# Performance work log

Hardware: AMD Instinct MI355X
Metric: run time of the kernel (lower is better)

## Reference

```python
import jax, jax.numpy as jnp
import numpy as np

PS = 3          # patch_size
ALPHA = 0.5     # alpha_0 (no step() calls -> stays at init value)
A_CUBIC = -0.75 # torch bicubic kernel coefficient


def _cubic_w(t):
    at = jnp.abs(t)
    w1 = ((A_CUBIC + 2.0) * at - (A_CUBIC + 3.0)) * at * at + 1.0
    w2 = A_CUBIC * (((at - 5.0) * at + 8.0) * at - 4.0)
    return jnp.where(at <= 1.0, w1, jnp.where(at < 2.0, w2, 0.0))


def _resize_axis(x, out_size, axis):
    # bicubic, align_corners=True, border-clamped (matches torch.nn.functional.interpolate)
    in_size = x.shape[axis]
    scale = (in_size - 1) / (out_size - 1)
    coords = jnp.arange(out_size, dtype=x.dtype) * jnp.asarray(scale, x.dtype)
    i0 = jnp.floor(coords)
    frac = coords - i0
    offs = jnp.arange(-1, 3)
    idx = jnp.clip(i0.astype(jnp.int32)[:, None] + offs[None, :], 0, in_size - 1)
    w = _cubic_w(frac[:, None] - offs[None, :].astype(x.dtype))  # [out,4]
    xm = jnp.moveaxis(x, axis, -1)
    vals = xm[..., idx]                      # [..., out, 4]
    out = jnp.einsum('...ot,ot->...o', vals, w)
    return jnp.moveaxis(out, -1, axis)


def _bicubic(x, out_h, out_w):
    return _resize_axis(_resize_axis(x, out_h, 2), out_w, 3)


def _unfold(x, ps=PS):
    # [B,C,H,W] -> [B, (H/ps)*(W/ps), C, ps, ps], row-major over (H-chunk, W-chunk)
    B, C, H, W = x.shape
    x = x.reshape(B, C, H // ps, ps, W // ps, ps)
    x = x.transpose(0, 2, 4, 1, 3, 5)
    return x.reshape(B, -1, C, ps, ps)


def _fold(p, C, H, W, ps=PS):
    B = p.shape[0]
    x = p.reshape(B, H // ps, W // ps, C, ps, ps)
    x = x.transpose(0, 3, 1, 4, 2, 5)
    return x.reshape(B, C, H, W)


def _g_database(tar, ps=PS):
    B, C, H, W = tar.shape
    scales = [tar, _bicubic(tar, H // 2, W // 2), _bicubic(tar, H // 4, W // 4)]
    patches = []
    for i in range(1, ps):
        for j in range(1, ps):
            for s in scales:
                h, w = s.shape[2], s.shape[3]
                if ps < min(h, w):
                    patches.append(_unfold(s[:, :, i:h - (ps - i), j:w - (ps - j)], ps))
    for s in scales:
        patches.append(_unfold(s, ps))
    return jnp.concatenate(patches, axis=1)  # [B, G, C, ps, ps]


def setup_inputs() -> dict:
    key = jax.random.key(0)
    k1, k2 = jax.random.split(key)
    inp = jax.random.uniform(k1, (2, 3, 144, 144), dtype=jnp.float32)
    tar = jax.random.uniform(k2, (2, 3, 144, 144), dtype=jnp.float32)
    return {"inp": inp, "tar": tar}


def reference(inp, tar):
    B, C, H, W = tar.shape
    ps = PS
    D = C * ps * ps
    ipf = _unfold(inp, ps).reshape(B, -1, D)   # [B,N,D]
    tpf = _unfold(tar, ps).reshape(B, -1, D)
    gf = _g_database(tar, ps).reshape(B, -1, D)  # [B,G,D]

    # nearest-candidate selection is done under no_grad in the original
    gf_s = jax.lax.stop_gradient(gf)
    tpf_s = jax.lax.stop_gradient(tpf)
    ipf_s = jax.lax.stop_gradient(ipf)
    gn = jnp.sum(gf_s * gf_s, axis=-1)  # [B,G]

    def sqdist(a):  # sum of squared diffs over D: [B,G,N]
        an = jnp.sum(a * a, axis=-1)
        return an[:, None, :] + gn[:, :, None] - 2.0 * jnp.einsum('bnd,bgd->bgn', a, gf_s)

    l = ALPHA * sqdist(tpf_s) + (1.0 - ALPHA) * sqdist(ipf_s)  # [B,G,N]
    index = jnp.argmin(l, axis=1)                              # [B,N]
    sel = jnp.take_along_axis(gf_s, index[..., None], axis=1)  # [B,N,D]

    loss_p = jnp.abs(ipf - sel)  # L1Loss(reduction='none')
    loss_img = _fold(loss_p.reshape(B, -1, C, ps, ps), C, H, W, ps)
    sel_img = _fold(sel.reshape(B, -1, C, ps, ps), C, H, W, ps)
    return loss_img.mean(), sel_img
```

## Files before the change

kernel.cpp:

```cpp
#include <hip/hip_runtime.h>
#include <math.h>

#define A_CUBIC (-0.75f)
#define NB 2
#define NC 3
#define HH 144
#define NPB 2304
#define GG 14460
#define DD 27
#define DP 28
#define GSPLIT 128
#define GTILE 113

typedef float v2f __attribute__((ext_vector_type(2)));

__constant__ int c_seg_start[15] = {0,2209,2738,2859,5068,5597,5718,7927,8456,8577,10786,11315,11436,13740,14316};
__constant__ int c_seg_gw[15]    = {47,23,11, 47,23,11, 47,23,11, 47,23,11, 48,24,12};
__constant__ int c_seg_oy[15]    = {1,1,1, 1,1,1, 2,2,2, 2,2,2, 0,0,0};
__constant__ int c_seg_ox[15]    = {1,1,1, 2,2,2, 1,1,1, 2,2,2, 0,0,0};
__constant__ int c_seg_src[15]   = {0,1,2, 0,1,2, 0,1,2, 0,1,2, 0,1,2};

__device__ __forceinline__ float cubicw(float t) {
    float at = fabsf(t);
    if (at <= 1.0f) return ((A_CUBIC + 2.0f) * at - (A_CUBIC + 3.0f)) * at * at + 1.0f;
    if (at < 2.0f)  return A_CUBIC * (((at - 5.0f) * at + 8.0f) * at - 4.0f);
    return 0.0f;
}

__global__ void prep_k(const float* __restrict__ tar, const float* __restrict__ inp,
                       float* __restrict__ s1, float* __restrict__ s2,
                       float* __restrict__ m, unsigned long long* __restrict__ best) {
    int t = blockIdx.x * 256 + threadIdx.x;
    const int total1 = NB * NC * 72 * 72;
    const int total2 = NB * NC * 36 * 36;
    if (t < total1 + total2) {
        float* dst; int O; int idx;
        if (t < total1) { dst = s1; O = 72; idx = t; }
        else            { dst = s2; O = 36; idx = t - total1; }
        int x  = idx % O;
        int y  = (idx / O) % O;
        int bc = idx / (O * O);
        const float* src = tar + (size_t)bc * HH * HH;
        float scale = (float)(143.0 / (double)(O - 1));
        float fy = (float)y * scale;
        float iyf = floorf(fy); float fry = fy - iyf; int iy = (int)iyf;
        float fx = (float)x * scale;
        float ixf = floorf(fx); float frx = fx - ixf; int ix = (int)ixf;
        float wy[4], wx[4];
        #pragma unroll
        for (int d = 0; d < 4; ++d) {
            wy[d] = cubicw(fry - (float)(d - 1));
            wx[d] = cubicw(frx - (float)(d - 1));
        }
        float acc = 0.0f;
        #pragma unroll
        for (int dx = 0; dx < 4; ++dx) {
            int cx = min(max(ix - 1 + dx, 0), HH - 1);
            float inner = 0.0f;
            #pragma unroll
            for (int dy = 0; dy < 4; ++dy) {
                int cy = min(max(iy - 1 + dy, 0), HH - 1);
                inner += wy[dy] * src[cy * HH + cx];
            }
            acc += wx[dx] * inner;
        }
        dst[idx] = acc;
    } else {
        int u = t - (total1 + total2);
        if (u >= NB * NPB) return;
        int b = u / NPB, n = u % NPB;
        int hc = n / 48, wc = n % 48;
        const float* ib = inp + (size_t)b * NC * HH * HH;
        const float* tb = tar + (size_t)b * NC * HH * HH;
        float* row = m + (size_t)u * DP;
        #pragma unroll
        for (int c = 0; c < 3; ++c)
            #pragma unroll
            for (int dy = 0; dy < 3; ++dy)
                #pragma unroll
                for (int dx = 0; dx < 3; ++dx) {
                    int off = (c * HH + hc * 3 + dy) * HH + wc * 3 + dx;
                    row[(c * 3 + dy) * 3 + dx] = ib[off] + tb[off];
                }
        row[27] = -1.0f;
        best[u] = 0ULL;
    }
}

__global__ void build_gf_k(const float* __restrict__ tar, const float* __restrict__ s1,
                           const float* __restrict__ s2, float* __restrict__ gf) {
    int t = blockIdx.x * 256 + threadIdx.x;
    if (t >= NB * GG) return;
    int b = t / GG, g = t % GG;
    int s = 0;
    #pragma unroll
    for (int k = 1; k < 15; ++k) if (g >= c_seg_start[k]) s = k;
    int p  = g - c_seg_start[s];
    int gw = c_seg_gw[s];
    int hc = p / gw, wc = p % gw;
    int oy = c_seg_oy[s], ox = c_seg_ox[s];
    int srci = c_seg_src[s];
    const float* img; int sz;
    if (srci == 0)      { img = tar; sz = 144; }
    else if (srci == 1) { img = s1;  sz = 72;  }
    else                { img = s2;  sz = 36;  }
    const float* base = img + (size_t)b * NC * sz * sz;
    int y0 = oy + hc * 3, x0 = ox + wc * 3;
    float acc = 0.0f;
    float* row = gf + (size_t)t * DP;
    #pragma unroll
    for (int c = 0; c < 3; ++c)
        #pragma unroll
        for (int dy = 0; dy < 3; ++dy)
            #pragma unroll
            for (int dx = 0; dx < 3; ++dx) {
                float v = base[((size_t)c * sz + y0 + dy) * sz + x0 + dx];
                row[(c * 3 + dy) * 3 + dx] = v;
                acc = fmaf(v, v, acc);
            }
    row[27] = acc;
}

__device__ __forceinline__ float dot28(const v2f mr[14], const v2f r[14]) {
    v2f a0 = {0.0f, 0.0f}, a1 = {0.0f, 0.0f};
    #pragma unroll
    for (int i = 0; i < 14; i += 2) {
        a0 = __builtin_elementwise_fma(mr[i],     r[i],     a0);
        a1 = __builtin_elementwise_fma(mr[i + 1], r[i + 1], a1);
    }
    v2f t = a0 + a1;
    return t.x + t.y;
}

__global__ __launch_bounds__(256, 8) void argmin_k(
        const float* __restrict__ gf, const float* __restrict__ m,
        unsigned long long* __restrict__ best) {
    int tid = threadIdx.x;
    int nblk = blockIdx.y;
    int b  = nblk / 9;
    int nn = nblk * 256 + tid;
    const v2f* mrow = (const v2f*)(m + (size_t)nn * DP);
    v2f mr[14];
    #pragma unroll
    for (int i = 0; i < 14; ++i) mr[i] = mrow[i];
    int g0 = blockIdx.x * GTILE;
    int g1 = min(g0 + GTILE, GG);
    const float* gfb = gf + (size_t)b * GG * DP;
    float bv = -3.0e38f; int bi = 0;

    v2f A[14], B[14];
    {
        const v2f* p = (const v2f*)(gfb + (size_t)g0 * DP);
        #pragma unroll
        for (int i = 0; i < 14; ++i) A[i] = p[i];
    }
    int g = g0;
    for (; g + 1 < g1; g += 2) {
        {
            const v2f* p = (const v2f*)(gfb + (size_t)(g + 1) * DP);
            #pragma unroll
            for (int i = 0; i < 14; ++i) B[i] = p[i];
        }
        float s = dot28(mr, A);
        if (s > bv) { bv = s; bi = g; }
        {
            const v2f* p = (const v2f*)(gfb + (size_t)(g + 2) * DP);
            #pragma unroll
            for (int i = 0; i < 14; ++i) A[i] = p[i];
        }
        float s2 = dot28(mr, B);
        if (s2 > bv) { bv = s2; bi = g + 1; }
    }
    if (g < g1) {
        float s = dot28(mr, A);
        if (s > bv) { bv = s; bi = g; }
    }
    unsigned u = __float_as_uint(bv);
    u ^= (unsigned)(((int)u >> 31)) | 0x80000000u;
    atomicMax(&best[nn], ((unsigned long long)u << 32) | (unsigned)(~bi));
}

__global__ void finalize_k(const float* __restrict__ gf,
                           const unsigned long long* __restrict__ best,
                           const float* __restrict__ inp,
                           float* __restrict__ out, float* __restrict__ lpart) {
    __shared__ float red[256];
    int t = blockIdx.x * 256 + threadIdx.x;
    float lsum = 0.0f;
    if (t < NB * NPB) {
        int b = t / NPB, n = t % NPB;
        unsigned long long pk = best[t];
        int bi = (int)(~(unsigned)(pk & 0xFFFFFFFFull));
        int hc = n / 48, wc = n % 48;
        const float* grow = gf + ((size_t)b * GG + bi) * DP;
        const float* ib   = inp + (size_t)b * NC * HH * HH;
        float* sel = out + 1 + (size_t)b * NC * HH * HH;
        #pragma unroll
        for (int c = 0; c < 3; ++c)
            #pragma unroll
            for (int dy = 0; dy < 3; ++dy)
                #pragma unroll
                for (int dx = 0; dx < 3; ++dx) {
                    int d = (c * 3 + dy) * 3 + dx;
                    float sv = grow[d];
                    int off = (c * HH + hc * 3 + dy) * HH + wc * 3 + dx;
                    sel[off] = sv;
                    lsum += fabsf(ib[off] - sv);
                }
    }
    red[threadIdx.x] = lsum;
    __syncthreads();
    for (int s = 128; s > 0; s >>= 1) {
        if (threadIdx.x < s) red[threadIdx.x] += red[threadIdx.x + s];
        __syncthreads();
    }
    if (threadIdx.x == 0) lpart[blockIdx.x] = red[0];
}

__global__ void sum_k(const float* __restrict__ lpart, float* __restrict__ out) {
    if (threadIdx.x == 0) {
        float s = 0.0f;
        for (int i = 0; i < 18; ++i) s += lpart[i];
        out[0] = s * (1.0f / 124416.0f);
    }
}

extern "C" void kernel_launch(void* const* d_in, const int* in_sizes, int n_in,
                              void* d_out, int out_size, void* d_ws, size_t ws_size,
                              hipStream_t stream) {
    const float* inp = (const float*)d_in[0];
    const float* tar = (const float*)d_in[1];
    float* out = (float*)d_out;
    float* ws  = (float*)d_ws;

    float* s1 = ws;
    float* s2 = s1 + 31104;
    float* gf = s2 + 7776;
    float* m  = gf + 809760;
    unsigned long long* best = (unsigned long long*)(m + 129024);
    float* lp = (float*)(best + 4608);

    prep_k    <<<(43488 + 255) / 256, 256, 0, stream>>>(tar, inp, s1, s2, m, best);
    build_gf_k<<<(28920 + 255) / 256, 256, 0, stream>>>(tar, s1, s2, gf);
    argmin_k  <<<dim3(GSPLIT, 18), 256, 0, stream>>>(gf, m, best);
    finalize_k<<<18, 256, 0, stream>>>(gf, best, inp, out, lp);
    sum_k     <<<1, 64, 0, stream>>>(lp, out);
}
```

Measured before the change: 79.94 us.

## Restructure argmin as shared-memory tiled GEMM with register blocking

The argmin kernel stops streaming each database row from global memory per thread. Instead, each block stages a 64-row query tile and 128-row database tiles, transposed, into LDS. Each thread then computes a 4x8 block of dot products from float4 LDS reads, keeps a running max per query, and a shared-memory reduction settles the winner per query before the atomic. To make the tiles uniform, the database is zero-padded to a multiple of 128 rows. This cuts redundant global/L1 traffic and raises arithmetic intensity, at the cost of block barriers and zero-padding rows that are only safe because real candidates always score higher.

```diff
diff --git a/kernel.cpp b/kernel.cpp
--- a/kernel.cpp
+++ b/kernel.cpp
@@ -7,12 +7,13 @@
 #define HH 144
 #define NPB 2304
 #define GG 14460
+#define GGP 14464
 #define DD 27
 #define DP 28
-#define GSPLIT 128
-#define GTILE 113
-
-typedef float v2f __attribute__((ext_vector_type(2)));
+#define NGT 113
+#define NSPLIT 16
+#define APAD 68
+#define BPAD 132
 
 __constant__ int c_seg_start[15] = {0,2209,2738,2859,5068,5597,5718,7927,8456,8577,10786,11315,11436,13740,14316};
 __constant__ int c_seg_gw[15]    = {47,23,11, 47,23,11, 47,23,11, 47,23,11, 48,24,12};
@@ -90,8 +91,14 @@
 __global__ void build_gf_k(const float* __restrict__ tar, const float* __restrict__ s1,
                            const float* __restrict__ s2, float* __restrict__ gf) {
     int t = blockIdx.x * 256 + threadIdx.x;
-    if (t >= NB * GG) return;
-    int b = t / GG, g = t % GG;
+    if (t >= NB * GGP) return;
+    int b = t / GGP, g = t % GGP;
+    float* row = gf + (size_t)t * DP;
+    if (g >= GG) {
+        #pragma unroll
+        for (int i = 0; i < DP; ++i) row[i] = 0.0f;
+        return;
+    }
     int s = 0;
     #pragma unroll
     for (int k = 1; k < 15; ++k) if (g >= c_seg_start[k]) s = k;
@@ -107,7 +114,6 @@
     const float* base = img + (size_t)b * NC * sz * sz;
     int y0 = oy + hc * 3, x0 = ox + wc * 3;
     float acc = 0.0f;
-    float* row = gf + (size_t)t * DP;
     #pragma unroll
     for (int c = 0; c < 3; ++c)
         #pragma unroll
@@ -121,63 +127,94 @@
     row[27] = acc;
 }
 
-__device__ __forceinline__ float dot28(const v2f mr[14], const v2f r[14]) {
-    v2f a0 = {0.0f, 0.0f}, a1 = {0.0f, 0.0f};
-    #pragma unroll
-    for (int i = 0; i < 14; i += 2) {
-        a0 = __builtin_elementwise_fma(mr[i],     r[i],     a0);
-        a1 = __builtin_elementwise_fma(mr[i + 1], r[i + 1], a1);
-    }
-    v2f t = a0 + a1;
-    return t.x + t.y;
-}
-
-__global__ __launch_bounds__(256, 8) void argmin_k(
+__global__ __launch_bounds__(256) void argmin_k(
         const float* __restrict__ gf, const float* __restrict__ m,
         unsigned long long* __restrict__ best) {
+    __shared__ __align__(16) float Al[28 * APAD];
+    __shared__ __align__(16) float Bl[28 * BPAD];
+    __shared__ float rv[64 * 17];
+    __shared__ int   ri[64 * 17];
     int tid = threadIdx.x;
-    int nblk = blockIdx.y;
-    int b  = nblk / 9;
-    int nn = nblk * 256 + tid;
-    const v2f* mrow = (const v2f*)(m + (size_t)nn * DP);
-    v2f mr[14];
-    #pragma unroll
-    for (int i = 0; i < 14; ++i) mr[i] = mrow[i];
-    int g0 = blockIdx.x * GTILE;
-    int g1 = min(g0 + GTILE, GG);
-    const float* gfb = gf + (size_t)b * GG * DP;
-    float bv = -3.0e38f; int bi = 0;
-
-    v2f A[14], B[14];
+    int tx = tid & 15;
+    int ty = tid >> 4;
+    int nt = blockIdx.y;
+    int n0 = nt * 64;
+    int b  = nt / 36;
+    int s  = blockIdx.x;
+    int t0 = (s * NGT) >> 4;
+    int t1 = ((s + 1) * NGT) >> 4;
+
     {
-        const v2f* p = (const v2f*)(gfb + (size_t)g0 * DP);
-        #pragma unroll
-        for (int i = 0; i < 14; ++i) A[i] = p[i];
-    }
-    int g = g0;
-    for (; g + 1 < g1; g += 2) {
+        const float* src = m + (size_t)n0 * DP;
+        for (int idx = tid; idx < 64 * DP; idx += 256) {
+            int r = idx / DP, k = idx - r * DP;
+            Al[k * APAD + r] = src[idx];
+        }
+    }
+
+    float bv[4]; int bi[4];
+    #pragma unroll
+    for (int i = 0; i < 4; ++i) { bv[i] = -3.0e38f; bi[i] = 0; }
+
+    const float* gbase = gf + (size_t)b * GGP * DP;
+    for (int t = t0; t < t1; ++t) {
+        __syncthreads();
         {
-            const v2f* p = (const v2f*)(gfb + (size_t)(g + 1) * DP);
-            #pragma unroll
-            for (int i = 0; i < 14; ++i) B[i] = p[i];
-        }
-        float s = dot28(mr, A);
-        if (s > bv) { bv = s; bi = g; }
-        {
-            const v2f* p = (const v2f*)(gfb + (size_t)(g + 2) * DP);
-            #pragma unroll
-            for (int i = 0; i < 14; ++i) A[i] = p[i];
-        }
-        float s2 = dot28(mr, B);
-        if (s2 > bv) { bv = s2; bi = g + 1; }
-    }
-    if (g < g1) {
-        float s = dot28(mr, A);
-        if (s > bv) { bv = s; bi = g; }
-    }
-    unsigned u = __float_as_uint(bv);
-    u ^= (unsigned)(((int)u >> 31)) | 0x80000000u;
-    atomicMax(&best[nn], ((unsigned long long)u << 32) | (unsigned)(~bi));
+            const float* src = gbase + (size_t)t * 128 * DP;
+            for (int idx = tid; idx < 128 * DP; idx += 256) {
+                int r = idx / DP, k = idx - r * DP;
+                Bl[k * BPAD + r] = src[idx];
+            }
+        }
+        __syncthreads();
+
+        float acc[4][8];
+        #pragma unroll
+        for (int i = 0; i < 4; ++i)
+            #pragma unroll
+            for (int j = 0; j < 8; ++j) acc[i][j] = 0.0f;
+
+        #pragma unroll
+        for (int k = 0; k < 28; ++k) {
+            float4 a  = *(const float4*)&Al[k * APAD + tx * 4];
+            float4 p  = *(const float4*)&Bl[k * BPAD + ty * 8];
+            float4 q  = *(const float4*)&Bl[k * BPAD + ty * 8 + 4];
+            float av[4] = {a.x, a.y, a.z, a.w};
+            float gv[8] = {p.x, p.y, p.z, p.w, q.x, q.y, q.z, q.w};
+            #pragma unroll
+            for (int i = 0; i < 4; ++i)
+                #pragma unroll
+                for (int j = 0; j < 8; ++j)
+                    acc[i][j] = fmaf(av[i], gv[j], acc[i][j]);
+        }
+
+        int gg0 = t * 128 + ty * 8;
+        #pragma unroll
+        for (int j = 0; j < 8; ++j) {
+            #pragma unroll
+            for (int i = 0; i < 4; ++i) {
+                if (acc[i][j] > bv[i]) { bv[i] = acc[i][j]; bi[i] = gg0 + j; }
+            }
+        }
+    }
+
+    #pragma unroll
+    for (int i = 0; i < 4; ++i) {
+        rv[(tx * 4 + i) * 17 + ty] = bv[i];
+        ri[(tx * 4 + i) * 17 + ty] = bi[i];
+    }
+    __syncthreads();
+    if (tid < 64) {
+        float v = -3.0e38f; int idx = 0x7fffffff;
+        #pragma unroll
+        for (int y = 0; y < 16; ++y) {
+            float vv = rv[tid * 17 + y]; int ii = ri[tid * 17 + y];
+            if (vv > v || (vv == v && ii < idx)) { v = vv; idx = ii; }
+        }
+        unsigned u = __float_as_uint(v);
+        u ^= (unsigned)(((int)u >> 31)) | 0x80000000u;
+        atomicMax(&best[n0 + tid], ((unsigned long long)u << 32) | (unsigned)(~idx));
+    }
 }
 
 __global__ void finalize_k(const float* __restrict__ gf,
@@ -192,7 +229,7 @@
         unsigned long long pk = best[t];
         int bi = (int)(~(unsigned)(pk & 0xFFFFFFFFull));
         int hc = n / 48, wc = n % 48;
-        const float* grow = gf + ((size_t)b * GG + bi) * DP;
+        const float* grow = gf + ((size_t)b * GGP + bi) * DP;
         const float* ib   = inp + (size_t)b * NC * HH * HH;
         float* sel = out + 1 + (size_t)b * NC * HH * HH;
         #pragma unroll
@@ -236,13 +273,13 @@
     float* s1 = ws;
     float* s2 = s1 + 31104;
     float* gf = s2 + 7776;
-    float* m  = gf + 809760;
+    float* m  = gf + 809984;
     unsigned long long* best = (unsigned long long*)(m + 129024);
     float* lp = (float*)(best + 4608);
 
     prep_k    <<<(43488 + 255) / 256, 256, 0, stream>>>(tar, inp, s1, s2, m, best);
-    build_gf_k<<<(28920 + 255) / 256, 256, 0, stream>>>(tar, s1, s2, gf);
-    argmin_k  <<<dim3(GSPLIT, 18), 256, 0, stream>>>(gf, m, best);
+    build_gf_k<<<(NB * GGP + 255) / 256, 256, 0, stream>>>(tar, s1, s2, gf);
+    argmin_k  <<<dim3(NSPLIT, 72), 256, 0, stream>>>(gf, m, best);
     finalize_k<<<18, 256, 0, stream>>>(gf, best, inp, out, lp);
     sum_k     <<<1, 64, 0, stream>>>(lp, out);
 }
```

New measurement: 87.66 us. 9.7% more time.
